# Performance work log

Hardware: AMD Instinct MI355X
Metric: run time of the kernel (lower is better)

## Reference

```python
import jax, jax.numpy as jnp
import numpy as np
from jax import lax

V, H, L, F = 50304, 512, 6, 2048
SKIP_INTERVAL = 1
B, S = 4, 1024


def layer_norm(x, w, b, eps=1e-5):
    mu = jnp.mean(x, axis=-1, keepdims=True)
    var = jnp.mean(jnp.square(x - mu), axis=-1, keepdims=True)
    return (x - mu) * lax.rsqrt(var + eps) * w + b


def setup_inputs() -> dict:
    key = jax.random.key(0)
    ks = jax.random.split(key, 8)
    s = 0.02
    return {
        "input_ids": jax.random.randint(ks[0], (B, S), 0, V, dtype=jnp.int64),
        "embed_in": jax.random.normal(ks[1], (V, H), jnp.float32) * s,
        "hp_w": jax.random.normal(ks[2], (H, H), jnp.float32) * s,
        "hp_b": jnp.zeros((H,), jnp.float32),
        "ln_w": jnp.ones((L, H), jnp.float32),
        "ln_b": jnp.zeros((L, H), jnp.float32),
        "W1": jax.random.normal(ks[3], (L, H, F), jnp.float32) * s,
        "b1": jnp.zeros((L, F), jnp.float32),
        "W2": jax.random.normal(ks[4], (L, F, H), jnp.float32) * s,
        "b2": jnp.zeros((L, H), jnp.float32),
        "ln_f_w": jnp.ones((H,), jnp.float32),
        "ln_f_b": jnp.zeros((H,), jnp.float32),
        "embed_out_w": jax.random.normal(ks[5], (V, H), jnp.float32) * s,
    }


def _stack(h, ln_w, ln_b, W1, b1, W2, b2):
    # scan over L layers; each is pre-LN residual MLP: h + gelu(LN(h) @ W1 + b1) @ W2 + b2
    def step(h, p):
        lw, lb, w1, bb1, w2, bb2 = p
        y = layer_norm(h, lw, lb)
        h = h + jnp.dot(jax.nn.gelu(jnp.dot(y, w1) + bb1), w2) + bb2
        return h, None
    h, _ = lax.scan(step, h, (ln_w, ln_b, W1, b1, W2, b2))
    return h


def reference(input_ids, embed_in, hp_w, hp_b, ln_w, ln_b, W1, b1, W2, b2, ln_f_w, ln_f_b, embed_out_w):
    # forward_selective with attention_mask=None and stateless layers is
    # position-independent, so the token loop vectorizes exactly to [B,S,H].
    h = embed_in[input_ids]  # [B,S,H] gather
    h = _stack(h, ln_w, ln_b, W1, b1, W2, b2)
    for _ in range(SKIP_INTERVAL):
        h = jnp.dot(h, hp_w.T) + hp_b  # hidden_proj
        h = _stack(h, ln_w, ln_b, W1, b1, W2, b2)
    normed = layer_norm(h, ln_f_w, ln_f_b)
    logits = jnp.dot(normed, embed_out_w.T)  # [B,S,V]
    final_hidden = h[:, -1, :]  # [B,H]
    return logits, final_hidden
```

## Files before the change

### kernel.cpp

```cpp
#include <hip/hip_runtime.h>
#include <hip/hip_bf16.h>
#include <cstdint>

using bf16 = __hip_bfloat16;
typedef __bf16 bf16x8 __attribute__((ext_vector_type(8)));
typedef float f32x4 __attribute__((ext_vector_type(4)));

constexpr int Hd = 512;
constexpr int Ld = 6;
constexpr int Fd = 2048;
constexpr int Vd = 50304;
constexpr int Md = 4096;

__device__ __forceinline__ unsigned short f2b(float x) {
  return __builtin_bit_cast(unsigned short, __float2bfloat16(x));
}

__device__ __forceinline__ float gelu_tanh(float x) {
  const float c = 0.7978845608028654f;
  float x3 = x * x * x;
  return 0.5f * x * (1.0f + tanhf(c * (x + 0.044715f * x3)));
}

__device__ __forceinline__ void load16_lds(const bf16* g, bf16* l) {
  __builtin_amdgcn_global_load_lds(
      (const __attribute__((address_space(1))) void*)g,
      (__attribute__((address_space(3))) void*)l, 16, 0, 0);
}

__global__ __launch_bounds__(256) void cast8(const float* __restrict__ in,
                                             bf16* __restrict__ out, int n8) {
  int i = blockIdx.x * 256 + threadIdx.x;
  if (i >= n8) return;
  const float4* p = (const float4*)in;
  float4 a = p[2 * i], b = p[2 * i + 1];
  uint4 o = {(unsigned)f2b(a.x) | ((unsigned)f2b(a.y) << 16),
             (unsigned)f2b(a.z) | ((unsigned)f2b(a.w) << 16),
             (unsigned)f2b(b.x) | ((unsigned)f2b(b.y) << 16),
             (unsigned)f2b(b.z) | ((unsigned)f2b(b.w) << 16)};
  ((uint4*)out)[i] = o;
}

__global__ void transpose_cast(const float* __restrict__ in, bf16* __restrict__ out,
                               int R, int C) {
  __shared__ float tile[32][33];
  int l = blockIdx.z;
  in += (size_t)l * R * C;
  out += (size_t)l * R * C;
  int c0 = blockIdx.x * 32, r0 = blockIdx.y * 32;
#pragma unroll
  for (int i = 0; i < 4; i++) {
    int r = r0 + threadIdx.y + i * 8;
    tile[threadIdx.y + i * 8][threadIdx.x] = in[(size_t)r * C + c0 + threadIdx.x];
  }
  __syncthreads();
#pragma unroll
  for (int i = 0; i < 4; i++) {
    int c = c0 + threadIdx.y + i * 8;
    out[(size_t)c * R + r0 + threadIdx.x] = (bf16)tile[threadIdx.x][threadIdx.y + i * 8];
  }
}

__global__ void gather_embed(const int* __restrict__ ids, const float* __restrict__ emb,
                             float* __restrict__ h) {
  int row = blockIdx.x;
  int id = ids[row];
  const float4* src = (const float4*)(emb + (size_t)id * Hd);
  float4* dst = (float4*)(h + (size_t)row * Hd);
  dst[threadIdx.x] = src[threadIdx.x];
}

template <int MODE>
__global__ __launch_bounds__(256) void ln_rows(
    const float* __restrict__ h, const float* __restrict__ p0,
    const float* __restrict__ p1, const float* __restrict__ fb,
    const float* __restrict__ w, const float* __restrict__ b,
    float* __restrict__ hout, bf16* __restrict__ y) {
  int row = blockIdx.x * 4 + (threadIdx.x >> 6);
  int lane = threadIdx.x & 63;
  size_t base = (size_t)row * Hd + lane * 8;
  float xv[8];
  if constexpr (MODE == 0) {
    *(float4*)&xv[0] = *(const float4*)(h + base);
    *(float4*)&xv[4] = *(const float4*)(h + base + 4);
  } else {
    float4 q0 = *(const float4*)(p0 + base), q1 = *(const float4*)(p0 + base + 4);
    float4 r0 = *(const float4*)(p1 + base), r1 = *(const float4*)(p1 + base + 4);
    float4 f0 = *(const float4*)(fb + lane * 8), f1 = *(const float4*)(fb + lane * 8 + 4);
    xv[0] = q0.x + r0.x + f0.x; xv[1] = q0.y + r0.y + f0.y;
    xv[2] = q0.z + r0.z + f0.z; xv[3] = q0.w + r0.w + f0.w;
    xv[4] = q1.x + r1.x + f1.x; xv[5] = q1.y + r1.y + f1.y;
    xv[6] = q1.z + r1.z + f1.z; xv[7] = q1.w + r1.w + f1.w;
    if constexpr (MODE == 1) {
      float4 a0 = *(const float4*)(h + base), a1 = *(const float4*)(h + base + 4);
      xv[0] += a0.x; xv[1] += a0.y; xv[2] += a0.z; xv[3] += a0.w;
      xv[4] += a1.x; xv[5] += a1.y; xv[6] += a1.z; xv[7] += a1.w;
    }
    *(float4*)(hout + base) = make_float4(xv[0], xv[1], xv[2], xv[3]);
    *(float4*)(hout + base + 4) = make_float4(xv[4], xv[5], xv[6], xv[7]);
  }
  float s = 0.f;
#pragma unroll
  for (int j = 0; j < 8; j++) s += xv[j];
#pragma unroll
  for (int off = 1; off < 64; off <<= 1) s += __shfl_xor(s, off);
  float mu = s * (1.0f / 512.0f);
  float s2 = 0.f;
#pragma unroll
  for (int j = 0; j < 8; j++) {
    xv[j] -= mu;
    s2 += xv[j] * xv[j];
  }
#pragma unroll
  for (int off = 1; off < 64; off <<= 1) s2 += __shfl_xor(s2, off);
  float scale = rsqrtf(s2 * (1.0f / 512.0f) + 1e-5f);
  float o[8];
#pragma unroll
  for (int j = 0; j < 8; j++) {
    float wj = w[lane * 8 + j], bj = b[lane * 8 + j];
    o[j] = xv[j] * scale * wj + bj;
  }
  uint4 pk = {(unsigned)f2b(o[0]) | ((unsigned)f2b(o[1]) << 16),
              (unsigned)f2b(o[2]) | ((unsigned)f2b(o[3]) << 16),
              (unsigned)f2b(o[4]) | ((unsigned)f2b(o[5]) << 16),
              (unsigned)f2b(o[6]) | ((unsigned)f2b(o[7]) << 16)};
  *(uint4*)(y + base) = pk;
}

__global__ __launch_bounds__(256) void finish2(
    const float* __restrict__ p0, const float* __restrict__ p1,
    const float* __restrict__ fb, float* __restrict__ h, bf16* __restrict__ hbf) {
  int i = blockIdx.x * 256 + threadIdx.x;
  size_t base = (size_t)i * 8;
  int col = (int)(base & 511);
  float x[8];
#pragma unroll
  for (int j = 0; j < 8; j += 4) {
    float4 a = *(const float4*)(h + base + j);
    float4 q = *(const float4*)(p0 + base + j);
    float4 r = *(const float4*)(p1 + base + j);
    float4 f = *(const float4*)(fb + col + j);
    x[j] = a.x + q.x + r.x + f.x; x[j + 1] = a.y + q.y + r.y + f.y;
    x[j + 2] = a.z + q.z + r.z + f.z; x[j + 3] = a.w + q.w + r.w + f.w;
    *(float4*)(h + base + j) = make_float4(x[j], x[j + 1], x[j + 2], x[j + 3]);
  }
  uint4 pk = {(unsigned)f2b(x[0]) | ((unsigned)f2b(x[1]) << 16),
              (unsigned)f2b(x[2]) | ((unsigned)f2b(x[3]) << 16),
              (unsigned)f2b(x[4]) | ((unsigned)f2b(x[5]) << 16),
              (unsigned)f2b(x[6]) | ((unsigned)f2b(x[7]) << 16)};
  *(uint4*)(hbf + base) = pk;
}

template <int EPI, int BN, bool MSWZ>
__global__ __launch_bounds__(256) void gemm_bt(
    const bf16* __restrict__ A, const bf16* __restrict__ Bt,
    const float* __restrict__ bias, float* __restrict__ outF,
    bf16* __restrict__ outB, int M, int N, int Klen, int lda, int ldb) {
  constexpr int ASZ = 128 * 32;
  constexpr int BSZ = BN * 32;
  constexpr int TILE = ASZ + BSZ;
  __shared__ bf16 lds[2 * TILE];
  const int tid = threadIdx.x;
  const int wave = tid >> 6;
  const int lane = tid & 63;
  constexpr int NF = BN / 32;
  const int wm = (wave >> 1) * 64;
  const int wn = (wave & 1) * (BN / 2);

  int bm, bn;
  if constexpr (MSWZ) {
    const int per = gridDim.x >> 3;
    const int wg = (blockIdx.x & 7) * per + (blockIdx.x >> 3);
    const int nM = M >> 7;
    bm = wg & (nM - 1);
    bn = wg / nM;
  } else {
    bn = blockIdx.x;
    bm = blockIdx.y;
  }
  const int rowA0 = bm * 128;
  const int rowB0 = bn * BN;
  const int k0 = blockIdx.z * Klen;

  const bf16* srcA[2];
#pragma unroll
  for (int r = 0; r < 2; r++) {
    int c = (r * 4 + wave) * 64 + lane;
    srcA[r] = A + (size_t)(rowA0 + (c >> 2)) * lda + k0 + (c & 3) * 8;
  }
  const bf16* srcB[BN / 64];
#pragma unroll
  for (int r = 0; r < BN / 64; r++) {
    int c = (r * 4 + wave) * 64 + lane;
    srcB[r] = Bt + (size_t)(rowB0 + (c >> 2)) * ldb + k0 + (c & 3) * 8;
  }

  f32x4 acc[4][NF];
#pragma unroll
  for (int i = 0; i < 4; i++)
#pragma unroll
    for (int j = 0; j < NF; j++) acc[i][j] = (f32x4){0.f, 0.f, 0.f, 0.f};

  const int fr = lane & 15;
  const int ko = (lane >> 4) * 8;

  auto STAGE = [&](int buf) {
    bf16* dst = lds + buf * TILE;
#pragma unroll
    for (int r = 0; r < 2; r++) {
      load16_lds(srcA[r], dst + (r * 4 + wave) * 512);
      srcA[r] += 32;
    }
#pragma unroll
    for (int r = 0; r < BN / 64; r++) {
      load16_lds(srcB[r], dst + ASZ + (r * 4 + wave) * 512);
      srcB[r] += 32;
    }
  };

  STAGE(0);
  __syncthreads();
  const int nIter = Klen >> 5;
  for (int it = 0; it < nIter; ++it) {
    const int cur = it & 1;
    if (it + 1 < nIter) STAGE(cur ^ 1);
    const bf16* lA = lds + cur * TILE;
    const bf16* lB = lA + ASZ;
    bf16x8 af[4], bfr[NF];
#pragma unroll
    for (int f = 0; f < 4; f++)
      af[f] = *(const bf16x8*)(lA + (wm + f * 16 + fr) * 32 + ko);
#pragma unroll
    for (int f = 0; f < NF; f++)
      bfr[f] = *(const bf16x8*)(lB + (wn + f * 16 + fr) * 32 + ko);
#pragma unroll
    for (int i = 0; i < 4; i++)
#pragma unroll
      for (int j = 0; j < NF; j++)
        acc[i][j] = __builtin_amdgcn_mfma_f32_16x16x32_bf16(af[i], bfr[j], acc[i][j], 0, 0, 0);
    __syncthreads();
  }

  if constexpr (EPI == 4) outF += (size_t)blockIdx.z * M * N;
  const int orow = (lane >> 4) * 4;
  const int ocol = lane & 15;
#pragma unroll
  for (int i = 0; i < 4; i++) {
#pragma unroll
    for (int j = 0; j < NF; j++) {
      int row0 = rowA0 + wm + i * 16 + orow;
      int col = rowB0 + wn + j * 16 + ocol;
#pragma unroll
      for (int q = 0; q < 4; q++) {
        float v = acc[i][j][q];
        size_t idx = (size_t)(row0 + q) * N + col;
        if constexpr (EPI == 0) {
          outB[idx] = (bf16)gelu_tanh(v + bias[col]);
        } else {
          outF[idx] = v;
        }
      }
    }
  }
}

__global__ void tail_copy(const float* __restrict__ h, float* __restrict__ out) {
  int t = blockIdx.x * 256 + threadIdx.x;
  int b = t >> 9, k = t & 511;
  out[t] = h[((size_t)(b * 1024 + 1023)) * Hd + k];
}

extern "C" void kernel_launch(void* const* d_in, const int* in_sizes, int n_in,
                              void* d_out, int out_size, void* d_ws, size_t ws_size,
                              hipStream_t stream) {
  const int* ids = (const int*)d_in[0];
  const float* emb = (const float*)d_in[1];
  const float* hp_w = (const float*)d_in[2];
  const float* hp_b = (const float*)d_in[3];
  const float* ln_w = (const float*)d_in[4];
  const float* ln_b = (const float*)d_in[5];
  const float* W1 = (const float*)d_in[6];
  const float* b1 = (const float*)d_in[7];
  const float* W2 = (const float*)d_in[8];
  const float* b2 = (const float*)d_in[9];
  const float* lnf_w = (const float*)d_in[10];
  const float* lnf_b = (const float*)d_in[11];
  const float* eow = (const float*)d_in[12];
  float* out = (float*)d_out;

  char* ws = (char*)d_ws;
  float* h = (float*)(ws);
  bf16* ybf = (bf16*)(ws + (8u << 20));
  bf16* abf = (bf16*)(ws + (12u << 20));
  bf16* W1t = (bf16*)(ws + (28u << 20));
  bf16* W2t = (bf16*)(ws + (40u << 20));
  bf16* hpwB = (bf16*)(ws + (52u << 20));
  bf16* eowB = (bf16*)(ws + (53u << 20));

  float* p0 = out;
  float* p1 = out + (size_t)Md * Hd;

  cast8<<<dim3(Vd * Hd / 8 / 256), dim3(256), 0, stream>>>(eow, eowB, Vd * Hd / 8);
  cast8<<<dim3(Hd * Hd / 8 / 256), dim3(256), 0, stream>>>(hp_w, hpwB, Hd * Hd / 8);
  transpose_cast<<<dim3(Fd / 32, Hd / 32, Ld), dim3(32, 8), 0, stream>>>(W1, W1t, Hd, Fd);
  transpose_cast<<<dim3(Hd / 32, Fd / 32, Ld), dim3(32, 8), 0, stream>>>(W2, W2t, Fd, Hd);

  gather_embed<<<dim3(Md), dim3(128), 0, stream>>>(ids, emb, h);

  auto layer = [&](int l, int mode, const float* fb, const float* lw, const float* lb) {
    if (mode == 0)
      ln_rows<0><<<dim3(Md / 4), dim3(256), 0, stream>>>(h, p0, p1, fb, lw, lb, h, ybf);
    else if (mode == 1)
      ln_rows<1><<<dim3(Md / 4), dim3(256), 0, stream>>>(h, p0, p1, fb, lw, lb, h, ybf);
    else
      ln_rows<2><<<dim3(Md / 4), dim3(256), 0, stream>>>(h, p0, p1, fb, lw, lb, h, ybf);
    gemm_bt<0, 128, false><<<dim3(Fd / 128, Md / 128), dim3(256), 0, stream>>>(
        ybf, W1t + (size_t)l * Fd * Hd, b1 + (size_t)l * Fd, (float*)nullptr, abf,
        Md, Fd, Hd, Hd, Hd);
    gemm_bt<4, 64, false><<<dim3(Hd / 64, Md / 128, 2), dim3(256), 0, stream>>>(
        abf, W2t + (size_t)l * Hd * Fd, (const float*)nullptr, p0, (bf16*)nullptr,
        Md, Hd, Fd / 2, Fd, Fd);
  };

  layer(0, 0, nullptr, ln_w, ln_b);
  for (int l = 1; l < Ld; l++)
    layer(l, 1, b2 + (size_t)(l - 1) * Hd, ln_w + (size_t)l * Hd, ln_b + (size_t)l * Hd);
  finish2<<<dim3(Md * Hd / 8 / 256), dim3(256), 0, stream>>>(
      p0, p1, b2 + (size_t)(Ld - 1) * Hd, h, ybf);

  gemm_bt<4, 64, false><<<dim3(Hd / 64, Md / 128, 2), dim3(256), 0, stream>>>(
      ybf, hpwB, (const float*)nullptr, p0, (bf16*)nullptr, Md, Hd, Hd / 2, Hd, Hd);

  layer(0, 2, hp_b, ln_w, ln_b);
  for (int l = 1; l < Ld; l++)
    layer(l, 1, b2 + (size_t)(l - 1) * Hd, ln_w + (size_t)l * Hd, ln_b + (size_t)l * Hd);

  ln_rows<1><<<dim3(Md / 4), dim3(256), 0, stream>>>(
      h, p0, p1, b2 + (size_t)(Ld - 1) * Hd, lnf_w, lnf_b, h, ybf);
  gemm_bt<3, 128, true><<<dim3((Vd / 128) * (Md / 128)), dim3(256), 0, stream>>>(
      ybf, eowB, (const float*)nullptr, out, (bf16*)nullptr, Md, Vd, Hd, Hd, Hd);

  tail_copy<<<dim3(8), dim3(256), 0, stream>>>(h, out + (size_t)Md * Vd);
}
```

Baseline: 1.099 ms.

## Add 256x128-tile 512-thread GEMM for W1 and vocab projection

Adds a new GEMM kernel with a 256x128 output tile, 8 waves of 512 threads, and double-buffered LDS staging. It replaces the 128x128 GEMM in the W1/GELU step and in the large logits projection. The larger M tile halves how often each B tile is reloaded and raises arithmetic intensity. In exchange it uses more LDS, issues fewer blocks, and may lower occupancy.

```diff
diff --git a/kernel.cpp b/kernel.cpp
--- a/kernel.cpp
+++ b/kernel.cpp
@@ -264,6 +264,109 @@
   }
 }
 
+template <int EPI, bool MSWZ>
+__global__ __launch_bounds__(512) void gemm_bt256(
+    const bf16* __restrict__ A, const bf16* __restrict__ Bt,
+    const float* __restrict__ bias, float* __restrict__ outF,
+    bf16* __restrict__ outB, int M, int N, int lda, int ldb) {
+  constexpr int ASZ = 256 * 32;
+  constexpr int BSZ = 128 * 32;
+  constexpr int TILE = ASZ + BSZ;
+  __shared__ bf16 lds[2 * TILE];
+  const int tid = threadIdx.x;
+  const int wave = tid >> 6;
+  const int lane = tid & 63;
+  const int wm = (wave >> 1) * 64;
+  const int wn = (wave & 1) * 64;
+
+  int bm, bn;
+  if constexpr (MSWZ) {
+    const int per = gridDim.x >> 3;
+    const int wg = (blockIdx.x & 7) * per + (blockIdx.x >> 3);
+    const int nM = M >> 8;
+    bm = wg & (nM - 1);
+    bn = wg / nM;
+  } else {
+    bn = blockIdx.x;
+    bm = blockIdx.y;
+  }
+  const int rowA0 = bm * 256;
+  const int rowB0 = bn * 128;
+
+  const bf16* srcA[2];
+#pragma unroll
+  for (int r = 0; r < 2; r++) {
+    int c = r * 512 + tid;
+    srcA[r] = A + (size_t)(rowA0 + (c >> 2)) * lda + (c & 3) * 8;
+  }
+  int cB = tid;
+  const bf16* srcB = Bt + (size_t)(rowB0 + (cB >> 2)) * ldb + (cB & 3) * 8;
+
+  f32x4 acc[4][4];
+#pragma unroll
+  for (int i = 0; i < 4; i++)
+#pragma unroll
+    for (int j = 0; j < 4; j++) acc[i][j] = (f32x4){0.f, 0.f, 0.f, 0.f};
+
+  const int fr = lane & 15;
+  const int ko = (lane >> 4) * 8;
+
+  auto STAGE = [&](int buf) {
+    bf16* dst = lds + buf * TILE;
+#pragma unroll
+    for (int r = 0; r < 2; r++) {
+      load16_lds(srcA[r], dst + (r * 512 + tid) * 8);
+      srcA[r] += 32;
+    }
+    load16_lds(srcB, dst + ASZ + tid * 8);
+    srcB += 32;
+  };
+
+  STAGE(0);
+  __syncthreads();
+  const int nIter = 512 >> 5;
+  for (int it = 0; it < nIter; ++it) {
+    const int cur = it & 1;
+    if (it + 1 < nIter) STAGE(cur ^ 1);
+    const bf16* lA = lds + cur * TILE;
+    const bf16* lB = lA + ASZ;
+    bf16x8 af[4], bfr[4];
+#pragma unroll
+    for (int f = 0; f < 4; f++)
+      af[f] = *(const bf16x8*)(lA + (wm + f * 16 + fr) * 32 + ko);
+#pragma unroll
+    for (int f = 0; f < 4; f++)
+      bfr[f] = *(const bf16x8*)(lB + (wn + f * 16 + fr) * 32 + ko);
+#pragma unroll
+    for (int i = 0; i < 4; i++)
+#pragma unroll
+      for (int j = 0; j < 4; j++)
+        acc[i][j] = __builtin_amdgcn_mfma_f32_16x16x32_bf16(af[i], bfr[j], acc[i][j], 0, 0, 0);
+    __syncthreads();
+  }
+
+  const int orow = (lane >> 4) * 4;
+  const int ocol = lane & 15;
+#pragma unroll
+  for (int i = 0; i < 4; i++) {
+#pragma unroll
+    for (int j = 0; j < 4; j++) {
+      int row0 = rowA0 + wm + i * 16 + orow;
+      int col = rowB0 + wn + j * 16 + ocol;
+#pragma unroll
+      for (int q = 0; q < 4; q++) {
+        float v = acc[i][j][q];
+        size_t idx = (size_t)(row0 + q) * N + col;
+        if constexpr (EPI == 0) {
+          outB[idx] = (bf16)gelu_tanh(v + bias[col]);
+        } else {
+          outF[idx] = v;
+        }
+      }
+    }
+  }
+}
+
 __global__ void tail_copy(const float* __restrict__ h, float* __restrict__ out) {
   int t = blockIdx.x * 256 + threadIdx.x;
   int b = t >> 9, k = t & 511;
@@ -314,9 +417,9 @@
       ln_rows<1><<<dim3(Md / 4), dim3(256), 0, stream>>>(h, p0, p1, fb, lw, lb, h, ybf);
     else
       ln_rows<2><<<dim3(Md / 4), dim3(256), 0, stream>>>(h, p0, p1, fb, lw, lb, h, ybf);
-    gemm_bt<0, 128, false><<<dim3(Fd / 128, Md / 128), dim3(256), 0, stream>>>(
+    gemm_bt256<0, false><<<dim3(Fd / 128, Md / 256), dim3(512), 0, stream>>>(
         ybf, W1t + (size_t)l * Fd * Hd, b1 + (size_t)l * Fd, (float*)nullptr, abf,
-        Md, Fd, Hd, Hd, Hd);
+        Md, Fd, Hd, Hd);
     gemm_bt<4, 64, false><<<dim3(Hd / 64, Md / 128, 2), dim3(256), 0, stream>>>(
         abf, W2t + (size_t)l * Hd * Fd, (const float*)nullptr, p0, (bf16*)nullptr,
         Md, Hd, Fd / 2, Fd, Fd);
@@ -337,8 +440,8 @@
 
   ln_rows<1><<<dim3(Md / 4), dim3(256), 0, stream>>>(
       h, p0, p1, b2 + (size_t)(Ld - 1) * Hd, lnf_w, lnf_b, h, ybf);
-  gemm_bt<3, 128, true><<<dim3((Vd / 128) * (Md / 128)), dim3(256), 0, stream>>>(
-      ybf, eowB, (const float*)nullptr, out, (bf16*)nullptr, Md, Vd, Hd, Hd, Hd);
+  gemm_bt256<3, true><<<dim3((Vd / 128) * (Md / 256)), dim3(512), 0, stream>>>(
+      ybf, eowB, (const float*)nullptr, out, (bf16*)nullptr, Md, Vd, Hd, Hd);
 
   tail_copy<<<dim3(8), dim3(256), 0, stream>>>(h, out + (size_t)Md * Vd);
 }
```

Measured after the change: 1.092 ms. About the same (-0.7%).
